# Kernel tuning notes

Hardware: AMD Instinct MI355X
Metric: run time of the kernel (lower is better)

## Reference

```python
import jax, jax.numpy as jnp
import numpy as np

H = 16          # num_attention_heads
D_MODEL = 2048  # hidden_size
HEAD_DIM = D_MODEL // H  # 128
B, S = 4, 2048


def setup_inputs() -> dict:
    key = jax.random.key(0)
    ks = jax.random.split(key, 9)
    std = D_MODEL ** -0.5
    hidden_states = jax.random.normal(ks[0], (B, S, D_MODEL), dtype=jnp.float32)
    q_w = jax.random.normal(ks[1], (H * HEAD_DIM, D_MODEL), dtype=jnp.float32) * std
    k_w = jax.random.normal(ks[2], (HEAD_DIM, D_MODEL), dtype=jnp.float32) * std
    v_w = jax.random.normal(ks[3], (HEAD_DIM, D_MODEL), dtype=jnp.float32) * std
    o_w = jax.random.normal(ks[4], (D_MODEL, H * HEAD_DIM), dtype=jnp.float32) * std
    q_b = jnp.zeros((H * HEAD_DIM,), dtype=jnp.float32)
    k_b = jnp.zeros((HEAD_DIM,), dtype=jnp.float32)
    v_b = jnp.zeros((HEAD_DIM,), dtype=jnp.float32)
    o_b = jnp.zeros((D_MODEL,), dtype=jnp.float32)
    return {"hidden_states": hidden_states, "q_w": q_w, "q_b": q_b,
            "k_w": k_w, "k_b": k_b, "v_w": v_w, "v_b": v_b,
            "o_w": o_w, "o_b": o_b}


def reference(hidden_states, q_w, q_b, k_w, k_b, v_w, v_b, o_w, o_b):
    b, s, _ = hidden_states.shape
    # projections: q -> H heads, k/v -> single shared KV head (MQA)
    q = (hidden_states @ q_w.T + q_b).reshape(b, s, H, HEAD_DIM)   # bshd
    k = hidden_states @ k_w.T + k_b                                 # bkd (1 kv head)
    v = hidden_states @ v_w.T + v_b                                 # bkd
    # QK^T with KV head broadcast across all query heads
    scores = jnp.einsum('bqhd,bkd->bhqk', q, k) / (HEAD_DIM ** 0.5)
    # causal mask (triu above diagonal)
    causal = jnp.triu(jnp.ones((s, s), dtype=bool), k=1)
    scores = jnp.where(causal[None, None], -jnp.inf, scores)
    # softmax in fp32, cast back to input dtype
    attn = jax.nn.softmax(scores.astype(jnp.float32), axis=-1).astype(q.dtype)
    out = jnp.einsum('bhqk,bkd->bqhd', attn, v).reshape(b, s, H * HEAD_DIM)
    return out @ o_w.T + o_b
```

## Files before the change

### kernel.cpp

```cpp
#include <hip/hip_runtime.h>
#include <stdint.h>

typedef __bf16 bf16;
typedef __bf16 bf16x4 __attribute__((ext_vector_type(4)));
typedef __bf16 bf16x8 __attribute__((ext_vector_type(8)));
typedef float f32x4 __attribute__((ext_vector_type(4)));

using gp_t = __attribute__((address_space(1))) const void*;
using lp_t = __attribute__((address_space(3))) void*;

__device__ __forceinline__ void gld16(const void* g, void* l) {
  __builtin_amdgcn_global_load_lds((gp_t)g, (lp_t)l, 16, 0, 0);
}

struct CvtSegs {
  const float* src[10];
  bf16* dst[10];
  int cnt[10];
  int n;
};

__global__ void cvt_kernel(CvtSegs segs) {
  const int stride = gridDim.x * blockDim.x;
  const int t0 = blockIdx.x * blockDim.x + threadIdx.x;
  for (int s = 0; s < segs.n; s++) {
    const float4* src = (const float4*)segs.src[s];
    bf16x4* dst = (bf16x4*)segs.dst[s];
    int cnt4 = segs.cnt[s] >> 2;
    for (int idx = t0; idx < cnt4; idx += stride) {
      float4 v = src[idx];
      bf16x4 o; o[0] = (bf16)v.x; o[1] = (bf16)v.y; o[2] = (bf16)v.z; o[3] = (bf16)v.w;
      dst[idx] = o;
    }
  }
}

__global__ __launch_bounds__(256, 2)
void gemm_bt(const bf16* __restrict__ A, const void* __restrict__ Wv,
             const void* __restrict__ biasv, void* __restrict__ Cv,
             int M, int N, int K, int w_fp32, int bias_fp32, int store_sel)
{
  __shared__ __align__(16) bf16 As[128 * 64];
  __shared__ __align__(16) bf16 Bs[128 * 64];
  const int tid  = threadIdx.x;
  const int lane = tid & 63;
  const int w    = tid >> 6;
  const int wm   = w >> 1, wn = w & 1;
  const int quad = lane >> 4, l16 = lane & 15;
  const int m0 = blockIdx.x * 128, n0 = blockIdx.y * 128;

  f32x4 acc[4][4] = {};

  for (int k0 = 0; k0 < K; k0 += 64) {
#pragma unroll
    for (int it = 0; it < 4; it++) {
      int c = tid + it * 256;
      int row = c >> 3;
      int cc  = (c & 7) ^ (row & 7);
      gld16(A + (size_t)(m0 + row) * K + k0 + cc * 8, &As[c * 8]);
      size_t woff = (size_t)(n0 + row) * K + k0 + cc * 8;
      if (!w_fp32) {
        gld16((const bf16*)Wv + woff, &Bs[c * 8]);
      } else {
        const float* Wf = (const float*)Wv;
        float4 x0 = *(const float4*)(Wf + woff);
        float4 x1 = *(const float4*)(Wf + woff + 4);
        bf16x8 v;
        v[0] = (bf16)x0.x; v[1] = (bf16)x0.y; v[2] = (bf16)x0.z; v[3] = (bf16)x0.w;
        v[4] = (bf16)x1.x; v[5] = (bf16)x1.y; v[6] = (bf16)x1.z; v[7] = (bf16)x1.w;
        *(bf16x8*)&Bs[c * 8] = v;
      }
    }
    __syncthreads();
#pragma unroll
    for (int dk = 0; dk < 2; dk++) {
      bf16x8 af[4], bw[4];
#pragma unroll
      for (int i = 0; i < 4; i++) {
        int row = wm * 64 + i * 16 + l16;
        af[i] = *(const bf16x8*)&As[(row * 8 + ((dk * 4 + quad) ^ (row & 7))) * 8];
      }
#pragma unroll
      for (int j = 0; j < 4; j++) {
        int row = wn * 64 + j * 16 + l16;
        bw[j] = *(const bf16x8*)&Bs[(row * 8 + ((dk * 4 + quad) ^ (row & 7))) * 8];
      }
#pragma unroll
      for (int i = 0; i < 4; i++)
#pragma unroll
        for (int j = 0; j < 4; j++)
          acc[i][j] = __builtin_amdgcn_mfma_f32_16x16x32_bf16(af[i], bw[j], acc[i][j], 0, 0, 0);
    }
    __syncthreads();
  }

#pragma unroll
  for (int j = 0; j < 4; j++) {
    int col = n0 + wn * 64 + j * 16 + l16;
    float bv = bias_fp32 ? ((const float*)biasv)[col] : (float)((const bf16*)biasv)[col];
#pragma unroll
    for (int i = 0; i < 4; i++) {
#pragma unroll
      for (int r = 0; r < 4; r++) {
        int row = m0 + wm * 64 + i * 16 + quad * 4 + r;
        float v = acc[i][j][r] + bv;
        if (store_sel == 0) {
          ((bf16*)Cv)[(size_t)row * N + col] = (bf16)v;
        } else if (store_sel == 2) {
          ((float*)Cv)[(size_t)row * N + col] = v;
        } else {
          int b = row >> 11, s = row & 2047;
          if (col < 128) {
            ((bf16*)Cv)[(size_t)row * 128 + col] = (bf16)v;
          } else {
            ((bf16*)Cv + 1048576)[((size_t)(b * 128 + (col - 128))) * 2048 + s] = (bf16)v;
          }
        }
      }
    }
  }
}

__global__ __launch_bounds__(256, 2)
void mqa_attn(const bf16* Qg, const bf16* __restrict__ Kg,
              const bf16* __restrict__ Vtg, bf16* AO)
{
  __shared__ __align__(16) bf16 Ks[64 * 128];
  __shared__ __align__(16) bf16 Vs[128 * 64];
  __shared__ __align__(16) bf16 Ps[4 * 32 * 64];

  const int tid  = threadIdx.x;
  const int lane = tid & 63;
  const int w    = tid >> 6;
  const int quad = lane >> 4, l16 = lane & 15;
  const int rb   = w * 32;
  const int pbase = w * 2048;
  const int bh = blockIdx.y;
  const int b  = bh >> 4, h = bh & 15;
  const float scale = 0.08838834764831845f;
  const float NEG = -3.0e4f;

  for (int half = 0; half < 2; half++) {
    const int qi = half ? (15 - (int)blockIdx.x) : (int)blockIdx.x;
    const int q0 = qi * 128;

    bf16x8 aq[2][4];
    {
      const bf16* qb = Qg + ((size_t)(b * 2048 + q0 + rb + l16)) * 2048 + h * 128 + quad * 8;
#pragma unroll
      for (int i = 0; i < 2; i++)
#pragma unroll
        for (int dk = 0; dk < 4; dk++)
          aq[i][dk] = *(const bf16x8*)(qb + (size_t)i * 16 * 2048 + dk * 32);
    }

    float m_reg[2][4], l_reg[2][4];
#pragma unroll
    for (int i = 0; i < 2; i++)
#pragma unroll
      for (int r = 0; r < 4; r++) { m_reg[i][r] = NEG; l_reg[i][r] = 0.0f; }

    f32x4 o[2][8] = {};

    const int ntiles = 2 * qi + 2;
    for (int kt = 0; kt < ntiles; kt++) {
      const int kk0 = kt * 64;
#pragma unroll
      for (int it = 0; it < 4; it++) {
        int c = tid + it * 256;
        int rk = c >> 4, ck = (c & 15) ^ (rk & 15);
        gld16(Kg + ((size_t)(b * 2048 + kk0 + rk)) * 128 + ck * 8, &Ks[c * 8]);
        int rv = c >> 3, cv = (c & 7) ^ (rv & 7);
        gld16(Vtg + ((size_t)(b * 128 + rv)) * 2048 + kk0 + cv * 8, &Vs[c * 8]);
      }
      __syncthreads();

      if (kk0 <= q0 + rb + 31) {
        f32x4 s[2][4] = {};
#pragma unroll
        for (int dk = 0; dk < 4; dk++) {
          bf16x8 bk[4];
#pragma unroll
          for (int j = 0; j < 4; j++) {
            int row = j * 16 + l16;
            bk[j] = *(const bf16x8*)&Ks[(row * 16 + ((dk * 4 + quad) ^ (row & 15))) * 8];
          }
#pragma unroll
          for (int i = 0; i < 2; i++)
#pragma unroll
            for (int j = 0; j < 4; j++)
              s[i][j] = __builtin_amdgcn_mfma_f32_16x16x32_bf16(aq[i][dk], bk[j], s[i][j], 0, 0, 0);
        }

        const bool masked_tile = (kk0 + 63 > q0 + rb);
#pragma unroll
        for (int i = 0; i < 2; i++)
#pragma unroll
          for (int j = 0; j < 4; j++)
#pragma unroll
            for (int r = 0; r < 4; r++) {
              float v = s[i][j][r] * scale;
              if (masked_tile) {
                int rg = q0 + rb + i * 16 + quad * 4 + r;
                int cg = kk0 + j * 16 + l16;
                if (cg > rg) v = NEG;
              }
              s[i][j][r] = v;
            }

#pragma unroll
        for (int i = 0; i < 2; i++)
#pragma unroll
          for (int r = 0; r < 4; r++) {
            float mx = fmaxf(fmaxf(s[i][0][r], s[i][1][r]), fmaxf(s[i][2][r], s[i][3][r]));
#pragma unroll
            for (int t = 1; t < 16; t <<= 1) mx = fmaxf(mx, __shfl_xor(mx, t, 64));
            float mo = m_reg[i][r];
            float mn = fmaxf(mo, mx);
            float alpha = __expf(mo - mn);
            int row = i * 16 + quad * 4 + r;
            float rs = 0.0f;
#pragma unroll
            for (int j = 0; j < 4; j++) {
              float p = __expf(s[i][j][r] - mn);
              rs += p;
              int col = j * 16 + l16;
              Ps[pbase + (row * 8 + ((col >> 3) ^ (row & 7))) * 8 + (col & 7)] = (bf16)p;
            }
#pragma unroll
            for (int t = 1; t < 16; t <<= 1) rs += __shfl_xor(rs, t, 64);
            l_reg[i][r] = l_reg[i][r] * alpha + rs;
            m_reg[i][r] = mn;
#pragma unroll
            for (int j = 0; j < 8; j++) o[i][j][r] *= alpha;
          }

#pragma unroll
        for (int kkt = 0; kkt < 2; kkt++) {
          bf16x8 ap[2], bv[8];
#pragma unroll
          for (int i = 0; i < 2; i++) {
            int row = i * 16 + l16;
            ap[i] = *(const bf16x8*)&Ps[pbase + (row * 8 + ((kkt * 4 + quad) ^ (row & 7))) * 8];
          }
#pragma unroll
          for (int j = 0; j < 8; j++) {
            int row = j * 16 + l16;
            bv[j] = *(const bf16x8*)&Vs[(row * 8 + ((kkt * 4 + quad) ^ (row & 7))) * 8];
          }
#pragma unroll
          for (int i = 0; i < 2; i++)
#pragma unroll
            for (int j = 0; j < 8; j++)
              o[i][j] = __builtin_amdgcn_mfma_f32_16x16x32_bf16(ap[i], bv[j], o[i][j], 0, 0, 0);
        }
      }
      __syncthreads();
    }

#pragma unroll
    for (int i = 0; i < 2; i++)
#pragma unroll
      for (int r = 0; r < 4; r++) {
        int row = rb + i * 16 + quad * 4 + r;
        float l = l_reg[i][r];
        float inv = (l > 0.0f) ? 1.0f / l : 0.0f;
        size_t base = ((size_t)(b * 2048 + q0 + row)) * 2048 + h * 128;
#pragma unroll
        for (int j = 0; j < 8; j++)
          AO[base + j * 16 + l16] = (bf16)(o[i][j][r] * inv);
      }
  }
}

extern "C" void kernel_launch(void* const* d_in, const int* in_sizes, int n_in,
                              void* d_out, int out_size, void* d_ws, size_t ws_size,
                              hipStream_t stream)
{
  const float* X   = (const float*)d_in[0];
  const float* q_w = (const float*)d_in[1];
  const float* q_b = (const float*)d_in[2];
  const float* k_w = (const float*)d_in[3];
  const float* k_b = (const float*)d_in[4];
  const float* v_w = (const float*)d_in[5];
  const float* v_b = (const float*)d_in[6];
  const float* o_w = (const float*)d_in[7];
  const float* o_b = (const float*)d_in[8];

  char* outc = (char*)d_out;
  bf16* Xb    = (bf16*)(outc);
  bf16* Kg    = (bf16*)(outc + 33554432);
  bf16* Vtg   = (bf16*)(outc + 35651584);
  bf16* wq_b  = (bf16*)(outc + 37748736);
  bf16* wkv_b = (bf16*)(outc + 46137344);
  bf16* qb_b  = (bf16*)(outc + 47185920);
  bf16* kvb_b = (bf16*)(outc + 47190016);

  bf16* Qg = (bf16*)d_ws;
  bf16* AO = Qg;

  const bool big_ws = ws_size >= (size_t)(33554432 + 8388608 + 8192);
  bf16* wo_b = big_ws ? (bf16*)((char*)d_ws + 33554432) : nullptr;
  bf16* ob_b = big_ws ? (bf16*)((char*)d_ws + 41943040) : nullptr;

  CvtSegs segs;
  int n = 0;
  segs.src[n] = X;   segs.dst[n] = Xb;            segs.cnt[n] = 16777216; n++;
  segs.src[n] = q_w; segs.dst[n] = wq_b;          segs.cnt[n] = 4194304;  n++;
  segs.src[n] = k_w; segs.dst[n] = wkv_b;         segs.cnt[n] = 262144;   n++;
  segs.src[n] = v_w; segs.dst[n] = wkv_b + 262144; segs.cnt[n] = 262144;  n++;
  segs.src[n] = q_b; segs.dst[n] = qb_b;          segs.cnt[n] = 2048;     n++;
  segs.src[n] = k_b; segs.dst[n] = kvb_b;         segs.cnt[n] = 128;      n++;
  segs.src[n] = v_b; segs.dst[n] = kvb_b + 128;   segs.cnt[n] = 128;      n++;
  if (big_ws) {
    segs.src[n] = o_w; segs.dst[n] = wo_b;        segs.cnt[n] = 4194304;  n++;
    segs.src[n] = o_b; segs.dst[n] = ob_b;        segs.cnt[n] = 2048;     n++;
  }
  segs.n = n;

  dim3 blk(256);
  cvt_kernel<<<dim3(1024), blk, 0, stream>>>(segs);
  gemm_bt<<<dim3(64, 16), blk, 0, stream>>>(Xb, wq_b, qb_b, Qg, 8192, 2048, 2048, 0, 0, 0);
  gemm_bt<<<dim3(64, 2),  blk, 0, stream>>>(Xb, wkv_b, kvb_b, Kg, 8192, 256, 2048, 0, 0, 3);
  mqa_attn<<<dim3(8, 64), blk, 0, stream>>>(Qg, Kg, Vtg, AO);
  if (big_ws)
    gemm_bt<<<dim3(64, 16), blk, 0, stream>>>(AO, wo_b, ob_b, d_out, 8192, 2048, 2048, 0, 0, 2);
  else
    gemm_bt<<<dim3(64, 16), blk, 0, stream>>>(AO, o_w, o_b, d_out, 8192, 2048, 2048, 1, 1, 2);
}
```

Baseline: 538.5 us.

## Double-buffer K/V tiles and keep attention probabilities in registers via transposed MFMA

The attention kernel now double-buffers the K/V tiles in shared memory, issuing the async loads for the next tile before computing on the current one, which removes the load-then-sync stall per tile. It computes S transposed (K as the A operand) so each lane holds a full query column. Probabilities can then feed the PV MFMA (16x16x16) directly from registers, removing the Ps shared-memory round trip. Softmax uses exp2 with a folded scale, reduces with fewer shuffles, skips the rescale when no lane's max grows, and writes the output as vector stores; the extra K/V buffer doubles that shared-memory use.

```diff
diff --git a/kernel.cpp b/kernel.cpp
--- a/kernel.cpp
+++ b/kernel.cpp
@@ -5,6 +5,7 @@
 typedef __bf16 bf16x4 __attribute__((ext_vector_type(4)));
 typedef __bf16 bf16x8 __attribute__((ext_vector_type(8)));
 typedef float f32x4 __attribute__((ext_vector_type(4)));
+typedef short s16x4 __attribute__((ext_vector_type(4)));
 
 using gp_t = __attribute__((address_space(1))) const void*;
 using lp_t = __attribute__((address_space(3))) void*;
@@ -125,19 +126,17 @@
 void mqa_attn(const bf16* Qg, const bf16* __restrict__ Kg,
               const bf16* __restrict__ Vtg, bf16* AO)
 {
-  __shared__ __align__(16) bf16 Ks[64 * 128];
-  __shared__ __align__(16) bf16 Vs[128 * 64];
-  __shared__ __align__(16) bf16 Ps[4 * 32 * 64];
+  __shared__ __align__(16) bf16 Ks[2][64 * 128];
+  __shared__ __align__(16) bf16 Vs[2][128 * 64];
 
   const int tid  = threadIdx.x;
   const int lane = tid & 63;
   const int w    = tid >> 6;
   const int quad = lane >> 4, l16 = lane & 15;
   const int rb   = w * 32;
-  const int pbase = w * 2048;
   const int bh = blockIdx.y;
   const int b  = bh >> 4, h = bh & 15;
-  const float scale = 0.08838834764831845f;
+  const float C2  = 0.12751879526288147f;
   const float NEG = -3.0e4f;
 
   for (int half = 0; half < 2; half++) {
@@ -154,122 +153,138 @@
           aq[i][dk] = *(const bf16x8*)(qb + (size_t)i * 16 * 2048 + dk * 32);
     }
 
-    float m_reg[2][4], l_reg[2][4];
-#pragma unroll
-    for (int i = 0; i < 2; i++)
-#pragma unroll
-      for (int r = 0; r < 4; r++) { m_reg[i][r] = NEG; l_reg[i][r] = 0.0f; }
-
-    f32x4 o[2][8] = {};
-
-    const int ntiles = 2 * qi + 2;
-    for (int kt = 0; kt < ntiles; kt++) {
+    float m_reg[2] = {NEG, NEG};
+    float l_reg[2] = {0.0f, 0.0f};
+    f32x4 ot[2][8] = {};
+
+    const int nt = 2 * qi + 2;
+
+#pragma unroll
+    for (int it = 0; it < 4; it++) {
+      int c = tid + it * 256;
+      int rk = c >> 4, ck = (c & 15) ^ (rk & 15);
+      gld16(Kg + ((size_t)(b * 2048 + rk)) * 128 + ck * 8, &Ks[0][c * 8]);
+      int rv = c >> 3, cv = (c & 7) ^ (rv & 7);
+      gld16(Vtg + ((size_t)(b * 128 + rv)) * 2048 + cv * 8, &Vs[0][c * 8]);
+    }
+    __syncthreads();
+
+    int cur = 0;
+    for (int kt = 0; kt < nt; kt++) {
       const int kk0 = kt * 64;
-#pragma unroll
-      for (int it = 0; it < 4; it++) {
-        int c = tid + it * 256;
-        int rk = c >> 4, ck = (c & 15) ^ (rk & 15);
-        gld16(Kg + ((size_t)(b * 2048 + kk0 + rk)) * 128 + ck * 8, &Ks[c * 8]);
-        int rv = c >> 3, cv = (c & 7) ^ (rv & 7);
-        gld16(Vtg + ((size_t)(b * 128 + rv)) * 2048 + kk0 + cv * 8, &Vs[c * 8]);
-      }
-      __syncthreads();
+
+      if (kt + 1 < nt) {
+        const int nk0 = kk0 + 64;
+#pragma unroll
+        for (int it = 0; it < 4; it++) {
+          int c = tid + it * 256;
+          int rk = c >> 4, ck = (c & 15) ^ (rk & 15);
+          gld16(Kg + ((size_t)(b * 2048 + nk0 + rk)) * 128 + ck * 8, &Ks[cur ^ 1][c * 8]);
+          int rv = c >> 3, cv = (c & 7) ^ (rv & 7);
+          gld16(Vtg + ((size_t)(b * 128 + rv)) * 2048 + nk0 + cv * 8, &Vs[cur ^ 1][c * 8]);
+        }
+      }
 
       if (kk0 <= q0 + rb + 31) {
-        f32x4 s[2][4] = {};
+        f32x4 st[4][2] = {};
 #pragma unroll
         for (int dk = 0; dk < 4; dk++) {
           bf16x8 bk[4];
 #pragma unroll
           for (int j = 0; j < 4; j++) {
             int row = j * 16 + l16;
-            bk[j] = *(const bf16x8*)&Ks[(row * 16 + ((dk * 4 + quad) ^ (row & 15))) * 8];
-          }
-#pragma unroll
-          for (int i = 0; i < 2; i++)
-#pragma unroll
-            for (int j = 0; j < 4; j++)
-              s[i][j] = __builtin_amdgcn_mfma_f32_16x16x32_bf16(aq[i][dk], bk[j], s[i][j], 0, 0, 0);
-        }
-
-        const bool masked_tile = (kk0 + 63 > q0 + rb);
-#pragma unroll
-        for (int i = 0; i < 2; i++)
+            bk[j] = *(const bf16x8*)&Ks[cur][(row * 16 + ((dk * 4 + quad) ^ (row & 15))) * 8];
+          }
 #pragma unroll
           for (int j = 0; j < 4; j++)
 #pragma unroll
-            for (int r = 0; r < 4; r++) {
-              float v = s[i][j][r] * scale;
-              if (masked_tile) {
-                int rg = q0 + rb + i * 16 + quad * 4 + r;
-                int cg = kk0 + j * 16 + l16;
-                if (cg > rg) v = NEG;
+            for (int i = 0; i < 2; i++)
+              st[j][i] = __builtin_amdgcn_mfma_f32_16x16x32_bf16(bk[j], aq[i][dk], st[j][i], 0, 0, 0);
+        }
+
+        if (kk0 + 63 > q0 + rb) {
+#pragma unroll
+          for (int j = 0; j < 4; j++)
+#pragma unroll
+            for (int i = 0; i < 2; i++)
+#pragma unroll
+              for (int r = 0; r < 4; r++) {
+                int key = kk0 + j * 16 + quad * 4 + r;
+                int qg  = q0 + rb + i * 16 + l16;
+                if (key > qg) st[j][i][r] = NEG;
               }
-              s[i][j][r] = v;
-            }
-
-#pragma unroll
-        for (int i = 0; i < 2; i++)
-#pragma unroll
-          for (int r = 0; r < 4; r++) {
-            float mx = fmaxf(fmaxf(s[i][0][r], s[i][1][r]), fmaxf(s[i][2][r], s[i][3][r]));
-#pragma unroll
-            for (int t = 1; t < 16; t <<= 1) mx = fmaxf(mx, __shfl_xor(mx, t, 64));
-            float mo = m_reg[i][r];
+        }
+
+        s16x4 ps[2][4];
+#pragma unroll
+        for (int i = 0; i < 2; i++) {
+          float mx = st[0][i][0];
+#pragma unroll
+          for (int j = 0; j < 4; j++)
+#pragma unroll
+            for (int r = 0; r < 4; r++) mx = fmaxf(mx, st[j][i][r]);
+          mx = fmaxf(mx, __shfl_xor(mx, 16, 64));
+          mx = fmaxf(mx, __shfl_xor(mx, 32, 64));
+          float mo = m_reg[i];
+          if (__any(mx > mo)) {
             float mn = fmaxf(mo, mx);
-            float alpha = __expf(mo - mn);
-            int row = i * 16 + quad * 4 + r;
-            float rs = 0.0f;
-#pragma unroll
-            for (int j = 0; j < 4; j++) {
-              float p = __expf(s[i][j][r] - mn);
-              rs += p;
-              int col = j * 16 + l16;
-              Ps[pbase + (row * 8 + ((col >> 3) ^ (row & 7))) * 8 + (col & 7)] = (bf16)p;
-            }
-#pragma unroll
-            for (int t = 1; t < 16; t <<= 1) rs += __shfl_xor(rs, t, 64);
-            l_reg[i][r] = l_reg[i][r] * alpha + rs;
-            m_reg[i][r] = mn;
-#pragma unroll
-            for (int j = 0; j < 8; j++) o[i][j][r] *= alpha;
-          }
-
-#pragma unroll
-        for (int kkt = 0; kkt < 2; kkt++) {
-          bf16x8 ap[2], bv[8];
-#pragma unroll
-          for (int i = 0; i < 2; i++) {
-            int row = i * 16 + l16;
-            ap[i] = *(const bf16x8*)&Ps[pbase + (row * 8 + ((kkt * 4 + quad) ^ (row & 7))) * 8];
-          }
-#pragma unroll
-          for (int j = 0; j < 8; j++) {
-            int row = j * 16 + l16;
-            bv[j] = *(const bf16x8*)&Vs[(row * 8 + ((kkt * 4 + quad) ^ (row & 7))) * 8];
-          }
-#pragma unroll
-          for (int i = 0; i < 2; i++)
-#pragma unroll
-            for (int j = 0; j < 8; j++)
-              o[i][j] = __builtin_amdgcn_mfma_f32_16x16x32_bf16(ap[i], bv[j], o[i][j], 0, 0, 0);
+            float al = exp2f((mo - mn) * C2);
+            l_reg[i] *= al;
+#pragma unroll
+            for (int jd = 0; jd < 8; jd++)
+#pragma unroll
+              for (int r = 0; r < 4; r++) ot[i][jd][r] *= al;
+            m_reg[i] = mn;
+          }
+          float mc = m_reg[i] * C2;
+          float rs = 0.0f;
+#pragma unroll
+          for (int j = 0; j < 4; j++) {
+            float p0 = exp2f(st[j][i][0] * C2 - mc);
+            float p1 = exp2f(st[j][i][1] * C2 - mc);
+            float p2 = exp2f(st[j][i][2] * C2 - mc);
+            float p3 = exp2f(st[j][i][3] * C2 - mc);
+            rs += (p0 + p1) + (p2 + p3);
+            union { bf16x4 h; s16x4 s; } pu;
+            pu.h[0] = (bf16)p0; pu.h[1] = (bf16)p1;
+            pu.h[2] = (bf16)p2; pu.h[3] = (bf16)p3;
+            ps[i][j] = pu.s;
+          }
+          rs += __shfl_xor(rs, 16, 64);
+          rs += __shfl_xor(rs, 32, 64);
+          l_reg[i] += rs;
+        }
+
+#pragma unroll
+        for (int jd = 0; jd < 8; jd++) {
+          int vrow = jd * 16 + l16;
+#pragma unroll
+          for (int jk = 0; jk < 4; jk++) {
+            int vch = (jk * 2 + (quad >> 1)) ^ (vrow & 7);
+            s16x4 vf = *(const s16x4*)&Vs[cur][(vrow * 8 + vch) * 8 + (quad & 1) * 4];
+#pragma unroll
+            for (int i = 0; i < 2; i++)
+              ot[i][jd] = __builtin_amdgcn_mfma_f32_16x16x16bf16_1k(vf, ps[i][jk], ot[i][jd], 0, 0, 0);
+          }
         }
       }
       __syncthreads();
-    }
-
-#pragma unroll
-    for (int i = 0; i < 2; i++)
-#pragma unroll
-      for (int r = 0; r < 4; r++) {
-        int row = rb + i * 16 + quad * 4 + r;
-        float l = l_reg[i][r];
-        float inv = (l > 0.0f) ? 1.0f / l : 0.0f;
-        size_t base = ((size_t)(b * 2048 + q0 + row)) * 2048 + h * 128;
-#pragma unroll
-        for (int j = 0; j < 8; j++)
-          AO[base + j * 16 + l16] = (bf16)(o[i][j][r] * inv);
-      }
+      cur ^= 1;
+    }
+
+#pragma unroll
+    for (int i = 0; i < 2; i++) {
+      float l = l_reg[i];
+      float inv = (l > 0.0f) ? 1.0f / l : 0.0f;
+      size_t base = ((size_t)(b * 2048 + q0 + rb + i * 16 + l16)) * 2048 + h * 128 + quad * 4;
+#pragma unroll
+      for (int jd = 0; jd < 8; jd++) {
+        bf16x4 ov;
+#pragma unroll
+        for (int r = 0; r < 4; r++) ov[r] = (bf16)(ot[i][jd][r] * inv);
+        *(bf16x4*)(AO + base + jd * 16) = ov;
+      }
+    }
   }
 }
 
```

Result: faster. 495.5 us (-8.0%).
